# Performance work log

Hardware: AMD Instinct MI355X
Metric: run time of the kernel (lower is better)

## Reference

```python
import jax, jax.numpy as jnp
import numpy as np

VOCAB = 100000
E = 300          # embedding_size
S = 128          # seq_len
B = 8192         # batch
H1 = 2048
H2 = 2048
C = 1221         # num_classes
PAD = 1          # padding token id (sentence trimmed after last non-1 token)


def setup_inputs() -> dict:
    key = jax.random.key(0)
    ks = jax.random.split(key, 8)
    x = jax.random.randint(ks[0], (S, B), 0, VOCAB, dtype=jnp.int64 if jax.config.jax_enable_x64 else jnp.int32)
    emb = jax.random.normal(ks[1], (VOCAB, E), dtype=jnp.float32) * 0.1
    W1 = jax.random.normal(ks[2], (H1, 2 * E), dtype=jnp.float32) * (1.0 / np.sqrt(2 * E))
    b1 = jnp.zeros((H1,), dtype=jnp.float32)
    W2 = jax.random.normal(ks[3], (H2, H1), dtype=jnp.float32) * (1.0 / np.sqrt(H1))
    b2 = jnp.zeros((H2,), dtype=jnp.float32)
    W_out = jax.random.normal(ks[4], (C, H2), dtype=jnp.float32) * (1.0 / np.sqrt(H2))
    b_out = jnp.zeros((C,), dtype=jnp.float32)
    return {"x": x, "emb": emb, "W1": W1, "b1": b1, "W2": W2, "b2": b2,
            "W_out": W_out, "b_out": b_out}


def reference(x, emb, W1, b1, W2, b2, W_out, b_out):
    # x: [S, B] token ids -> transpose to [B, S] as in torch forward
    xb = x.T                                   # [B, S]
    nonpad = xb != PAD                         # [B, S]
    # index of LAST non-padding token per sentence (torch: (sent != 1).nonzero()[-1])
    last = (S - 1) - jnp.argmax(nonpad[:, ::-1], axis=1)      # [B]
    pos = jnp.arange(S)
    # sentence[:last+1] keeps everything up to and including `last`,
    # including any PAD tokens inside that prefix (faithful to the slice).
    mask = (pos[None, :] <= last[:, None]).astype(emb.dtype)  # [B, S]

    ex = emb[xb]                               # [B, S, E] embedding lookup
    mean = jnp.einsum('bse,bs->be', ex, mask) / jnp.sum(mask, axis=1, keepdims=True)
    feat = jnp.concatenate([ex[:, 0, :], mean], axis=1)       # [B, 2E] (FEE + avg)

    h = jax.nn.relu(feat @ W1.T + b1)          # [B, H1]
    h = jax.nn.relu(h @ W2.T + b2)             # [B, H2]
    out = h @ W_out.T + b_out                  # [B, C]
    return out
```

## Files before the change

### kernel.cpp

```cpp
#include <hip/hip_runtime.h>
#include <hip/hip_bf16.h>

#define S 128
#define BATCH 8192
#define E 300
#define KPAD 640
#define H1 2048
#define H2 2048
#define CLS 1221
#define CPAD 1280
#define PADTOK 1
#define VOCAB 100000

typedef __bf16 bf16x8 __attribute__((ext_vector_type(8)));
typedef float f32x4 __attribute__((ext_vector_type(4)));

__device__ __forceinline__ float b2f(ushort u) {
  union { unsigned int i; float f; } v; v.i = ((unsigned int)u) << 16; return v.f;
}
__device__ __forceinline__ ushort f2b(float f) {
  unsigned int i = __float_as_uint(f);
  unsigned int r = (i + 0x7FFFu + ((i >> 16) & 1u)) >> 16;
  return (ushort)r;
}
__device__ __forceinline__ void async16(const void* g, void* l) {
  __builtin_amdgcn_global_load_lds(
      (__attribute__((address_space(1))) void*)(void*)(const_cast<void*>(g)),
      (__attribute__((address_space(3))) void*)l, 16, 0, 0);
}

#define NQ_EMB (VOCAB * E / 4)
#define NQ_W1  (H1 * KPAD / 4)
#define NQ_W2  (H1 * H2 / 4)
#define NQ_WO  (CPAD * H2 / 4)
#define NQ_XT  (S * BATCH / 4)
#define NQ_TOT (NQ_EMB + NQ_W1 + NQ_W2 + NQ_WO + NQ_XT)

__global__ __launch_bounds__(256) void cvt_all(const float* __restrict__ Ein,
                                               ushort* __restrict__ Eb,
                                               const float* __restrict__ W1,
                                               ushort* __restrict__ W1p,
                                               const float* __restrict__ W2,
                                               ushort* __restrict__ W2b,
                                               const float* __restrict__ Wout,
                                               ushort* __restrict__ Woutp,
                                               const int* __restrict__ x,
                                               int* __restrict__ xT) {
  int q = blockIdx.x * 256 + threadIdx.x;
  if (q < NQ_EMB) {
    float4 v = ((const float4*)Ein)[q];
    ushort4 o;
    o.x = f2b(v.x); o.y = f2b(v.y); o.z = f2b(v.z); o.w = f2b(v.w);
    ((ushort4*)Eb)[q] = o;
    return;
  }
  q -= NQ_EMB;
  if (q < NQ_W1) {
    int row = q / 160;
    int k0 = (q - row * 160) * 4;
    ushort4 o; o.x = 0; o.y = 0; o.z = 0; o.w = 0;
    if (k0 < 2 * E) {
      float4 v = *(const float4*)(W1 + (size_t)row * (2 * E) + k0);
      o.x = f2b(v.x); o.y = f2b(v.y); o.z = f2b(v.z); o.w = f2b(v.w);
    }
    ((ushort4*)W1p)[q] = o;
    return;
  }
  q -= NQ_W1;
  if (q < NQ_W2) {
    float4 v = ((const float4*)W2)[q];
    ushort4 o;
    o.x = f2b(v.x); o.y = f2b(v.y); o.z = f2b(v.z); o.w = f2b(v.w);
    ((ushort4*)W2b)[q] = o;
    return;
  }
  q -= NQ_W2;
  if (q < NQ_WO) {
    int n = (q * 4) >> 11;
    ushort4 o; o.x = 0; o.y = 0; o.z = 0; o.w = 0;
    if (n < CLS) {
      float4 v = ((const float4*)Wout)[q];
      o.x = f2b(v.x); o.y = f2b(v.y); o.z = f2b(v.z); o.w = f2b(v.w);
    }
    ((ushort4*)Woutp)[q] = o;
    return;
  }
  q -= NQ_WO;
  if (q < NQ_XT) {
    int b = q >> 5;
    int t4 = (q & 31) * 4;
    int4 o;
    o.x = x[(size_t)(t4 + 0) * BATCH + b];
    o.y = x[(size_t)(t4 + 1) * BATCH + b];
    o.z = x[(size_t)(t4 + 2) * BATCH + b];
    o.w = x[(size_t)(t4 + 3) * BATCH + b];
    ((int4*)xT)[q] = o;
  }
}

__global__ __launch_bounds__(128) void embed_kernel(const int* __restrict__ xT,
                                                    const ushort* __restrict__ emb,
                                                    ushort* __restrict__ feat) {
  __shared__ uint offs[S];
  __shared__ unsigned long long masks[2];
  __shared__ __align__(16) float part[76 * 4];
  const int b = blockIdx.x;
  const int t = threadIdx.x;

  int tok = xT[b * S + t];
  offs[t] = (uint)tok * 600u;
  unsigned long long m = __ballot(tok != PADTOK);
  if ((t & 63) == 0) masks[t >> 6] = m;
  __syncthreads();

  unsigned long long m0 = masks[0], m1 = masks[1];
  int last;
  if (m1)      last = 127 - __clzll(m1);
  else if (m0) last = 63 - __clzll(m0);
  else         last = S - 1;
  const int n = last + 1;
  const float inv = 1.0f / (float)n;

  const int w = t >> 6;
  const int lane = t & 63;
  const char* base = (const char*)emb;
  const uint off0 = (uint)lane * 8u;
  const bool tail = (lane < 11);
  const uint off1 = 512u + (uint)lane * 8u;

  float a0 = 0.f, a1 = 0.f, a2 = 0.f, a3 = 0.f;
  float c0 = 0.f, c1 = 0.f, c2 = 0.f, c3 = 0.f;

  int s = w;
  for (; s + 14 < n; s += 16) {
    uint o[8];
#pragma unroll
    for (int j = 0; j < 8; j++) o[j] = offs[s + 2 * j];
    ushort4 u[8];
#pragma unroll
    for (int j = 0; j < 8; j++) u[j] = *(const ushort4*)(base + (o[j] + off0));
    ushort4 v[8];
    if (tail) {
#pragma unroll
      for (int j = 0; j < 8; j++) v[j] = *(const ushort4*)(base + (o[j] + off1));
    }
#pragma unroll
    for (int j = 0; j < 8; j++) {
      a0 += b2f(u[j].x); a1 += b2f(u[j].y);
      a2 += b2f(u[j].z); a3 += b2f(u[j].w);
    }
    if (tail) {
#pragma unroll
      for (int j = 0; j < 8; j++) {
        c0 += b2f(v[j].x); c1 += b2f(v[j].y);
        c2 += b2f(v[j].z); c3 += b2f(v[j].w);
      }
    }
  }
  for (; s < n; s += 2) {
    uint o = offs[s];
    ushort4 u = *(const ushort4*)(base + (o + off0));
    a0 += b2f(u.x); a1 += b2f(u.y); a2 += b2f(u.z); a3 += b2f(u.w);
    if (tail) {
      ushort4 v = *(const ushort4*)(base + (o + off1));
      c0 += b2f(v.x); c1 += b2f(v.y); c2 += b2f(v.z); c3 += b2f(v.w);
    }
  }

  if (w == 1) {
    float4 av; av.x = a0; av.y = a1; av.z = a2; av.w = a3;
    *(float4*)&part[lane * 4] = av;
    if (tail) {
      float4 cv; cv.x = c0; cv.y = c1; cv.z = c2; cv.w = c3;
      *(float4*)&part[(64 + lane) * 4] = cv;
    }
  }
  __syncthreads();

  ushort* fr = feat + (size_t)b * KPAD;
  if (w == 0) {
    float4 pv = *(const float4*)&part[lane * 4];
    ushort4 mo;
    mo.x = f2b((a0 + pv.x) * inv); mo.y = f2b((a1 + pv.y) * inv);
    mo.z = f2b((a2 + pv.z) * inv); mo.w = f2b((a3 + pv.w) * inv);
    *(ushort4*)(fr + E + lane * 4) = mo;
    if (tail) {
      float4 qv = *(const float4*)&part[(64 + lane) * 4];
      ushort4 mo2;
      mo2.x = f2b((c0 + qv.x) * inv); mo2.y = f2b((c1 + qv.y) * inv);
      mo2.z = f2b((c2 + qv.z) * inv); mo2.w = f2b((c3 + qv.w) * inv);
      *(ushort4*)(fr + E + (64 + lane) * 4) = mo2;
    }
  }

  const uint o0 = offs[0];
  if (t < 75) {
    *(ushort4*)(fr + 4 * t) = *(const ushort4*)(base + (o0 + 8u * (uint)t));
  } else if (t < 85) {
    ushort4 z; z.x = 0; z.y = 0; z.z = 0; z.w = 0;
    *(ushort4*)(fr + 2 * E + 4 * (t - 75)) = z;
  }
}

#define BM2 256
#define BN2 256
#define BK2 32

__device__ __forceinline__ void stage32(const ushort* __restrict__ P,
                                        int ld, int org, ushort* dst,
                                        int kg, int tid, int wave) {
  const int sc = tid & 3;
  const int r0 = tid >> 2;
#pragma unroll
  for (int j = 0; j < 2; ++j) {
    const int row = j * 128 + r0;
    const int c2 = sc ^ ((row >> 1) & 3);
    async16(P + (size_t)(org + row) * ld + kg + c2 * 8,
            (void*)(dst + j * 4096 + wave * 512));
  }
}

#define PH_READ_B()                                                          \
  _Pragma("unroll") for (int nf = 0; nf < 4; ++nf) {                         \
    const int row = wc * 64 + nf * 16 + fr;                                  \
    bfrag[nf] = *(const bf16x8*)&sB[row * 32 +                               \
                                    ((fq ^ ((row >> 1) & 3)) * 8)];          \
  }
#define PH_READ_A(MH)                                                        \
  _Pragma("unroll") for (int f = 0; f < 4; ++f) {                            \
    const int row = wr * 128 + (MH) * 64 + f * 16 + fr;                      \
    afrag[f] = *(const bf16x8*)&sA[row * 32 +                                \
                                   ((fq ^ ((row >> 1) & 3)) * 8)];           \
  }
#define PH_MFMA(MH)                                                          \
  __builtin_amdgcn_s_setprio(1);                                             \
  _Pragma("unroll") for (int f = 0; f < 4; ++f)                              \
    _Pragma("unroll") for (int nf = 0; nf < 4; ++nf)                         \
      acc[(MH) * 4 + f][nf] = __builtin_amdgcn_mfma_f32_16x16x32_bf16(       \
          afrag[f], bfrag[nf], acc[(MH) * 4 + f][nf], 0, 0, 0);              \
  __builtin_amdgcn_s_setprio(0);
#define BAR_SCHED()                                                          \
  __builtin_amdgcn_s_barrier();                                              \
  __builtin_amdgcn_sched_barrier(0);

template <bool RELU, bool NGUARD, bool FP32OUT>
__global__ __launch_bounds__(512, 2) void gemm_bt(const ushort* __restrict__ A,
                                                  const ushort* __restrict__ B,
                                                  const float* __restrict__ bias,
                                                  void* __restrict__ Cv,
                                                  int K, int lda, int ldb,
                                                  int ldc, int Nreal) {
  __shared__ __align__(16) ushort sm[65536];

  const int tid = threadIdx.x;
  const int wave = tid >> 6;
  const int lane = tid & 63;

  const int gx = gridDim.x;
  const int nwg = gx * gridDim.y;
  const int lin = blockIdx.y * gx + blockIdx.x;
  const int wsw = (lin & 7) * (nwg >> 3) + (lin >> 3);
  const int m0 = (wsw / gx) * BM2;
  const int n0 = (wsw % gx) * BN2;

  const int wr = wave >> 2;
  const int wc = wave & 3;
  const int fr = lane & 15;
  const int fq = lane >> 4;

  f32x4 acc[8][4];
#pragma unroll
  for (int i = 0; i < 8; ++i)
#pragma unroll
    for (int j = 0; j < 4; ++j)
#pragma unroll
      for (int r = 0; r < 4; ++r) acc[i][j][r] = 0.f;

  bf16x8 afrag[4], bfrag[4];
  const int NT = K / BK2;

  {
    stage32(A, lda, m0, sm,                 0, tid, wave);
    stage32(B, ldb, n0, sm + 8192,          0, tid, wave);
    stage32(A, lda, m0, sm + 16384,        32, tid, wave);
    stage32(B, ldb, n0, sm + 16384 + 8192, 32, tid, wave);
    stage32(A, lda, m0, sm + 32768,        64, tid, wave);
    stage32(B, ldb, n0, sm + 32768 + 8192, 64, tid, wave);
    asm volatile("s_waitcnt vmcnt(8)" ::: "memory");
    BAR_SCHED();
  }

  for (int t = 0; t <= NT - 4; ++t) {
    const ushort* sA = sm + (t & 3) * 16384;
    const ushort* sB = sA + 8192;
    ushort* dst = sm + ((t + 3) & 3) * 16384;
    const int kn = (t + 3) * BK2;

    PH_READ_B();
    PH_READ_A(0);
    stage32(A, lda, m0, dst, kn, tid, wave);
    BAR_SCHED();
    PH_MFMA(0);
    BAR_SCHED();

    PH_READ_A(1);
    stage32(B, ldb, n0, dst + 8192, kn, tid, wave);
    asm volatile("s_waitcnt vmcnt(8)" ::: "memory");
    BAR_SCHED();
    PH_MFMA(1);
    BAR_SCHED();
  }

  {
    const ushort* sA = sm + ((NT - 3) & 3) * 16384;
    const ushort* sB = sA + 8192;
    PH_READ_B();
    PH_READ_A(0);
    BAR_SCHED();
    PH_MFMA(0);
    BAR_SCHED();
    PH_READ_A(1);
    asm volatile("s_waitcnt vmcnt(4)" ::: "memory");
    BAR_SCHED();
    PH_MFMA(1);
    BAR_SCHED();
  }
  {
    const ushort* sA = sm + ((NT - 2) & 3) * 16384;
    const ushort* sB = sA + 8192;
    PH_READ_B();
    PH_READ_A(0);
    BAR_SCHED();
    PH_MFMA(0);
    BAR_SCHED();
    PH_READ_A(1);
    asm volatile("s_waitcnt vmcnt(0)" ::: "memory");
    BAR_SCHED();
    PH_MFMA(1);
    BAR_SCHED();
  }
  {
    const ushort* sA = sm + ((NT - 1) & 3) * 16384;
    const ushort* sB = sA + 8192;
    PH_READ_B();
    PH_READ_A(0);
    BAR_SCHED();
    PH_MFMA(0);
    BAR_SCHED();
    PH_READ_A(1);
    PH_MFMA(1);
  }

#pragma unroll
  for (int nf = 0; nf < 4; ++nf) {
    const int col = n0 + wc * 64 + nf * 16 + fr;
    const bool ok = (!NGUARD) || (col < Nreal);
    const float bv = ok ? bias[col] : 0.f;
#pragma unroll
    for (int g = 0; g < 8; ++g) {
      const int rbase = m0 + wr * 128 + (g >> 2) * 64 + (g & 3) * 16 + fq * 4;
#pragma unroll
      for (int rr = 0; rr < 4; ++rr) {
        const int row = rbase + rr;
        float v = acc[g][nf][rr] + bv;
        if (RELU) v = fmaxf(v, 0.f);
        if (ok) {
          if (FP32OUT) ((float*)Cv)[(size_t)row * ldc + col] = v;
          else         ((ushort*)Cv)[(size_t)row * ldc + col] = f2b(v);
        }
      }
    }
  }
}

extern "C" void kernel_launch(void* const* d_in, const int* in_sizes, int n_in,
                              void* d_out, int out_size, void* d_ws, size_t ws_size,
                              hipStream_t stream) {
  const int* x = (const int*)d_in[0];
  const float* emb = (const float*)d_in[1];
  const float* W1 = (const float*)d_in[2];
  const float* b1 = (const float*)d_in[3];
  const float* W2 = (const float*)d_in[4];
  const float* b2 = (const float*)d_in[5];
  const float* Wout = (const float*)d_in[6];
  const float* bout = (const float*)d_in[7];
  float* out = (float*)d_out;

  char* ws = (char*)d_ws;
  ushort* feat = (ushort*)ws;  ws += (size_t)BATCH * KPAD * 2;
  ushort* h1 = (ushort*)ws;    ws += (size_t)BATCH * H1 * 2;
  ushort* h2 = (ushort*)ws;    ws += (size_t)BATCH * H2 * 2;
  ushort* W1p = (ushort*)ws;   ws += (size_t)H1 * KPAD * 2;
  ushort* W2b = (ushort*)ws;   ws += (size_t)H2 * H1 * 2;
  ushort* Woutp = (ushort*)ws; ws += (size_t)CPAD * H2 * 2;
  ushort* Eb = (ushort*)ws;    ws += (size_t)VOCAB * E * 2;
  int* xT = (int*)ws;          ws += (size_t)S * BATCH * 4;

  cvt_all<<<(NQ_TOT + 255) / 256, 256, 0, stream>>>(emb, Eb, W1, W1p, W2, W2b,
                                                    Wout, Woutp, x, xT);
  embed_kernel<<<BATCH, S, 0, stream>>>(xT, Eb, feat);

  gemm_bt<true, false, false><<<dim3(H1 / BN2, BATCH / BM2), 512, 0, stream>>>(
      feat, W1p, b1, (void*)h1, KPAD, KPAD, KPAD, H1, H1);
  gemm_bt<true, false, false><<<dim3(H2 / BN2, BATCH / BM2), 512, 0, stream>>>(
      h1, W2b, b2, (void*)h2, H1, H1, H1, H2, H2);
  gemm_bt<false, true, true><<<dim3(CPAD / BN2, BATCH / BM2), 512, 0, stream>>>(
      h2, Woutp, bout, (void*)out, H2, H2, H2, CLS, CLS);
}
```

Before: 490.9 us.

## Double-buffer GEMM LDS fragments in registers and merge global staging per iteration

Restructures the bf16 GEMM main loop so each iteration's MFMA phases overlap with LDS reads of the next tile's B and first-half A fragments. Alternating even/odd register sets hold those fragments, and the loop is unrolled by two. Both A and B global-to-LDS async copies are now issued together in one phase, which cuts block barriers per K-step from four to two. The aim is to hide LDS read latency and reduce synchronization stalls. The cost is extra fragment registers on top of a 128-register accumulator, which risks spills or lower occupancy.

Result: no change. 488.6 us (-0.5%).

```diff
diff --git a/kernel.cpp b/kernel.cpp
--- a/kernel.cpp
+++ b/kernel.cpp
@@ -220,28 +220,52 @@
   }
 }
 
-#define PH_READ_B()                                                          \
+#define RD_B(REG, SBASE)                                                     \
   _Pragma("unroll") for (int nf = 0; nf < 4; ++nf) {                         \
     const int row = wc * 64 + nf * 16 + fr;                                  \
-    bfrag[nf] = *(const bf16x8*)&sB[row * 32 +                               \
-                                    ((fq ^ ((row >> 1) & 3)) * 8)];          \
-  }
-#define PH_READ_A(MH)                                                        \
+    REG[nf] = *(const bf16x8*)&(SBASE)[row * 32 +                            \
+                                       ((fq ^ ((row >> 1) & 3)) * 8)];       \
+  }
+#define RD_A(REG, SBASE, MH)                                                 \
   _Pragma("unroll") for (int f = 0; f < 4; ++f) {                            \
     const int row = wr * 128 + (MH) * 64 + f * 16 + fr;                      \
-    afrag[f] = *(const bf16x8*)&sA[row * 32 +                                \
-                                   ((fq ^ ((row >> 1) & 3)) * 8)];           \
-  }
-#define PH_MFMA(MH)                                                          \
+    REG[f] = *(const bf16x8*)&(SBASE)[row * 32 +                             \
+                                      ((fq ^ ((row >> 1) & 3)) * 8)];        \
+  }
+#define MF(MH, RB, RA)                                                       \
   __builtin_amdgcn_s_setprio(1);                                             \
   _Pragma("unroll") for (int f = 0; f < 4; ++f)                              \
     _Pragma("unroll") for (int nf = 0; nf < 4; ++nf)                         \
       acc[(MH) * 4 + f][nf] = __builtin_amdgcn_mfma_f32_16x16x32_bf16(       \
-          afrag[f], bfrag[nf], acc[(MH) * 4 + f][nf], 0, 0, 0);              \
+          RA[f], RB[nf], acc[(MH) * 4 + f][nf], 0, 0, 0);                    \
   __builtin_amdgcn_s_setprio(0);
-#define BAR_SCHED()                                                          \
+#define SB0() __builtin_amdgcn_sched_barrier(0)
+#define BARS()                                                               \
   __builtin_amdgcn_s_barrier();                                              \
   __builtin_amdgcn_sched_barrier(0);
+
+#define STEADY_BODY(T, RB, RA0, RBN, RA0N)                                   \
+  {                                                                          \
+    const ushort* sA_c = sm + ((T) & 3) * 16384;                             \
+    RD_A(ra1, sA_c, 1);                                                      \
+    SB0();                                                                   \
+    MF(0, RB, RA0);                                                          \
+    BARS();                                                                  \
+    {                                                                        \
+      ushort* dstS = sm + (((T) + 3) & 3) * 16384;                           \
+      stage32(A, lda, m0, dstS, ((T) + 3) * BK2, tid, wave);                 \
+      stage32(B, ldb, n0, dstS + 8192, ((T) + 3) * BK2, tid, wave);          \
+    }                                                                        \
+    asm volatile("s_waitcnt vmcnt(8)" ::: "memory");                         \
+    BARS();                                                                  \
+    {                                                                        \
+      const ushort* sA_n = sm + (((T) + 1) & 3) * 16384;                     \
+      RD_B(RBN, sA_n + 8192);                                                \
+      RD_A(RA0N, sA_n, 0);                                                   \
+    }                                                                        \
+    SB0();                                                                   \
+    MF(1, RB, ra1);                                                          \
+  }
 
 template <bool RELU, bool NGUARD, bool FP32OUT>
 __global__ __launch_bounds__(512, 2) void gemm_bt(const ushort* __restrict__ A,
@@ -276,7 +300,7 @@
 #pragma unroll
       for (int r = 0; r < 4; ++r) acc[i][j][r] = 0.f;
 
-  bf16x8 afrag[4], bfrag[4];
+  bf16x8 rbE[4], ra0E[4], rbO[4], ra0O[4], ra1[4];
   const int NT = K / BK2;
 
   {
@@ -287,68 +311,52 @@
     stage32(A, lda, m0, sm + 32768,        64, tid, wave);
     stage32(B, ldb, n0, sm + 32768 + 8192, 64, tid, wave);
     asm volatile("s_waitcnt vmcnt(8)" ::: "memory");
-    BAR_SCHED();
-  }
-
-  for (int t = 0; t <= NT - 4; ++t) {
-    const ushort* sA = sm + (t & 3) * 16384;
-    const ushort* sB = sA + 8192;
-    ushort* dst = sm + ((t + 3) & 3) * 16384;
-    const int kn = (t + 3) * BK2;
-
-    PH_READ_B();
-    PH_READ_A(0);
-    stage32(A, lda, m0, dst, kn, tid, wave);
-    BAR_SCHED();
-    PH_MFMA(0);
-    BAR_SCHED();
-
-    PH_READ_A(1);
-    stage32(B, ldb, n0, dst + 8192, kn, tid, wave);
-    asm volatile("s_waitcnt vmcnt(8)" ::: "memory");
-    BAR_SCHED();
-    PH_MFMA(1);
-    BAR_SCHED();
-  }
+    BARS();
+    RD_B(rbE, sm + 8192);
+    RD_A(ra0E, sm, 0);
+  }
+
+  int t = 0;
+  for (; t + 1 <= NT - 4; t += 2) {
+    STEADY_BODY(t,     rbE, ra0E, rbO, ra0O);
+    STEADY_BODY(t + 1, rbO, ra0O, rbE, ra0E);
+  }
+  STEADY_BODY(t, rbE, ra0E, rbO, ra0O);
 
   {
-    const ushort* sA = sm + ((NT - 3) & 3) * 16384;
-    const ushort* sB = sA + 8192;
-    PH_READ_B();
-    PH_READ_A(0);
-    BAR_SCHED();
-    PH_MFMA(0);
-    BAR_SCHED();
-    PH_READ_A(1);
+    const ushort* sA_c = sm + ((NT - 3) & 3) * 16384;
+    RD_A(ra1, sA_c, 1);
+    SB0();
+    MF(0, rbO, ra0O);
+    BARS();
     asm volatile("s_waitcnt vmcnt(4)" ::: "memory");
-    BAR_SCHED();
-    PH_MFMA(1);
-    BAR_SCHED();
+    BARS();
+    const ushort* sA_n = sm + ((NT - 2) & 3) * 16384;
+    RD_B(rbE, sA_n + 8192);
+    RD_A(ra0E, sA_n, 0);
+    SB0();
+    MF(1, rbO, ra1);
   }
   {
-    const ushort* sA = sm + ((NT - 2) & 3) * 16384;
-    const ushort* sB = sA + 8192;
-    PH_READ_B();
-    PH_READ_A(0);
-    BAR_SCHED();
-    PH_MFMA(0);
-    BAR_SCHED();
-    PH_READ_A(1);
+    const ushort* sA_c = sm + ((NT - 2) & 3) * 16384;
+    RD_A(ra1, sA_c, 1);
+    SB0();
+    MF(0, rbE, ra0E);
+    BARS();
     asm volatile("s_waitcnt vmcnt(0)" ::: "memory");
-    BAR_SCHED();
-    PH_MFMA(1);
-    BAR_SCHED();
+    BARS();
+    const ushort* sA_n = sm + ((NT - 1) & 3) * 16384;
+    RD_B(rbO, sA_n + 8192);
+    RD_A(ra0O, sA_n, 0);
+    SB0();
+    MF(1, rbE, ra1);
   }
   {
-    const ushort* sA = sm + ((NT - 1) & 3) * 16384;
-    const ushort* sB = sA + 8192;
-    PH_READ_B();
-    PH_READ_A(0);
-    BAR_SCHED();
-    PH_MFMA(0);
-    BAR_SCHED();
-    PH_READ_A(1);
-    PH_MFMA(1);
+    const ushort* sA_c = sm + ((NT - 1) & 3) * 16384;
+    RD_A(ra1, sA_c, 1);
+    SB0();
+    MF(0, rbO, ra0O);
+    MF(1, rbO, ra1);
   }
 
 #pragma unroll
```
